# Kernel tuning notes

Measured on AMD Instinct MI355X. Metric: run time of the kernel, lower is better.

## Reference

```python
import jax, jax.numpy as jnp
import numpy as np

NUM_EXPERTS = 8
TOP_K = 2
EMB = 1024
HID = 2048


def setup_inputs() -> dict:
    key = jax.random.key(0)
    k1, k2, k3, k4, k5 = jax.random.split(key, 5)
    x = jax.random.normal(k1, (4, 4096, EMB), dtype=jnp.float32)
    router_w = jax.random.normal(k2, (EMB, NUM_EXPERTS), dtype=jnp.float32) * 0.02
    w_gate = jax.random.normal(k3, (NUM_EXPERTS, EMB, HID), dtype=jnp.float32) * 0.02
    w_up = jax.random.normal(k4, (NUM_EXPERTS, EMB, HID), dtype=jnp.float32) * 0.02
    w_down = jax.random.normal(k5, (NUM_EXPERTS, HID, EMB), dtype=jnp.float32) * 0.02
    return {"x": x, "router_w": router_w, "w_gate": w_gate, "w_up": w_up, "w_down": w_down}


def reference(x, router_w, w_gate, w_up, w_down):
    B, S, D = x.shape
    xf = x.reshape(-1, D)                      # [T, D]
    T = xf.shape[0]
    # Router: top-k over expert logits, softmax over the selected logits,
    # scattered back into a dense [T, E] weight matrix (zeros elsewhere).
    logits = xf @ router_w                     # [T, E]
    top_vals, top_idx = jax.lax.top_k(logits, TOP_K)
    top_probs = jax.nn.softmax(top_vals, axis=-1)
    weights = jnp.zeros((T, NUM_EXPERTS), dtype=xf.dtype)
    weights = weights.at[jnp.arange(T)[:, None], top_idx].set(top_probs)
    # Expert combine: since unselected experts have weight 0, summing the
    # weighted dense expert outputs equals the original masked dispatch/combine.
    out = jnp.zeros_like(xf)
    for e in range(NUM_EXPERTS):
        h = jax.nn.silu(xf @ w_gate[e]) * (xf @ w_up[e])   # SwiGLU [T, H]
        out = out + (h @ w_down[e]) * weights[:, e:e + 1]
    return out.reshape(B, S, D)
```

## Files before the change

### kernel.cpp

```cpp
#include <hip/hip_runtime.h>
#include <hip/hip_fp16.h>


#define T_TOK 16384
#define EMB_D 1024
#define HID_D 2048
#define NEXP  8
#define LIST_CAP (2 * T_TOK + 256)

typedef _Float16 f16x8 __attribute__((ext_vector_type(8)));
typedef _Float16 f16x4 __attribute__((ext_vector_type(4)));
typedef float    f32x4 __attribute__((ext_vector_type(4)));

#define GLD16(gp, lp)                                                          \
  __builtin_amdgcn_global_load_lds(                                            \
      (__attribute__((address_space(1))) void*)(void*)(gp),                    \
      (__attribute__((address_space(3))) void*)(lp), 16, 0, 0)

#define VMW(N)  asm volatile("s_waitcnt vmcnt(" #N ")" ::: "memory")
#define LGKM0() asm volatile("s_waitcnt lgkmcnt(0)" ::: "memory")

__global__ __launch_bounds__(256) void router_kernel(
    const float* __restrict__ x, const float* __restrict__ rw,
    _Float16* __restrict__ xh, int* __restrict__ top_idx,
    float2* __restrict__ top_w) {
  int wave = threadIdx.x >> 6, lane = threadIdx.x & 63;
  int tbase = (blockIdx.x * 4 + wave) * 4;

  float acc[4][NEXP];
#pragma unroll
  for (int tok = 0; tok < 4; tok++)
#pragma unroll
    for (int e = 0; e < NEXP; e++) acc[tok][e] = 0.f;

#pragma unroll
  for (int j = 0; j < 4; j++) {
    int d0 = j * 256 + lane * 4;
    const float* wr = rw + (size_t)d0 * NEXP;
    float wrf[4][NEXP];
#pragma unroll
    for (int k = 0; k < 4; k++) {
      float4 a = *(const float4*)(wr + k * NEXP);
      float4 b = *(const float4*)(wr + k * NEXP + 4);
      wrf[k][0] = a.x; wrf[k][1] = a.y; wrf[k][2] = a.z; wrf[k][3] = a.w;
      wrf[k][4] = b.x; wrf[k][5] = b.y; wrf[k][6] = b.z; wrf[k][7] = b.w;
    }
#pragma unroll
    for (int tok = 0; tok < 4; tok++) {
      int t = tbase + tok;
      float4 xv = *(const float4*)(x + (size_t)t * EMB_D + d0);
      float xs[4] = {xv.x, xv.y, xv.z, xv.w};
#pragma unroll
      for (int k = 0; k < 4; k++)
#pragma unroll
        for (int e = 0; e < NEXP; e++) acc[tok][e] += xs[k] * wrf[k][e];
      f16x4 hx;
      hx[0] = (_Float16)xv.x; hx[1] = (_Float16)xv.y;
      hx[2] = (_Float16)xv.z; hx[3] = (_Float16)xv.w;
      *(f16x4*)(xh + (size_t)t * EMB_D + d0) = hx;
    }
  }

#pragma unroll
  for (int off = 32; off > 0; off >>= 1)
#pragma unroll
    for (int tok = 0; tok < 4; tok++)
#pragma unroll
      for (int e = 0; e < NEXP; e++)
        acc[tok][e] += __shfl_xor(acc[tok][e], off, 64);

  if (lane == 0) {
#pragma unroll
    for (int tok = 0; tok < 4; tok++) {
      int t = tbase + tok;
      int i0 = 0; float v0 = acc[tok][0];
#pragma unroll
      for (int e = 1; e < NEXP; e++)
        if (acc[tok][e] > v0) { v0 = acc[tok][e]; i0 = e; }
      int i1 = (i0 == 0) ? 1 : 0; float v1 = acc[tok][i1];
#pragma unroll
      for (int e = 0; e < NEXP; e++)
        if (e != i0 && acc[tok][e] > v1) { v1 = acc[tok][e]; i1 = e; }
      float p = __expf(v1 - v0);
      float inv = 1.f / (1.f + p);
      top_idx[t] = i0 | (i1 << 16);
      top_w[t] = make_float2(inv, p * inv);
    }
  }
}

__global__ __launch_bounds__(256) void hist_kernel(
    const int* __restrict__ top_idx, int* __restrict__ counts) {
  __shared__ int wcnt[4][NEXP];
  int wave = threadIdx.x >> 6, lane = threadIdx.x & 63;
  int t = blockIdx.x * 256 + threadIdx.x;
  int pk = top_idx[t];
  int e0 = pk & 0xffff, e1 = pk >> 16;
#pragma unroll
  for (int e = 0; e < NEXP; e++) {
    unsigned long long m0 = __ballot(e0 == e);
    unsigned long long m1 = __ballot(e1 == e);
    if (lane == 0) wcnt[wave][e] = __popcll(m0) + __popcll(m1);
  }
  __syncthreads();
  if (threadIdx.x < NEXP) {
    int s = wcnt[0][threadIdx.x] + wcnt[1][threadIdx.x] +
            wcnt[2][threadIdx.x] + wcnt[3][threadIdx.x];
    atomicAdd(&counts[threadIdx.x], s);
  }
}

__global__ void scan_kernel(const int* __restrict__ counts,
                            int* __restrict__ offsets, int* __restrict__ cursor) {
  if (threadIdx.x == 0) {
    int s = 0;
    for (int e = 0; e < NEXP; e++) { offsets[e] = s; s += counts[e]; }
  }
  if (threadIdx.x < NEXP) cursor[threadIdx.x] = 0;
}

__global__ __launch_bounds__(256) void build_kernel(
    const int* __restrict__ top_idx, const float2* __restrict__ top_w,
    const int* __restrict__ offsets, int* cursor,
    int* __restrict__ list_token, float* __restrict__ list_w,
    int2* __restrict__ rows) {
  __shared__ int cnt[NEXP];
  __shared__ int basee[NEXP];
  int t = blockIdx.x * 256 + threadIdx.x;
  if (threadIdx.x < NEXP) cnt[threadIdx.x] = 0;
  __syncthreads();
  int pk = top_idx[t];
  float2 w = top_w[t];
  int e0 = pk & 0xffff, e1 = pk >> 16;
  int loc0 = atomicAdd(&cnt[e0], 1);
  int loc1 = atomicAdd(&cnt[e1], 1);
  __syncthreads();
  if (threadIdx.x < NEXP)
    basee[threadIdx.x] = atomicAdd(&cursor[threadIdx.x], cnt[threadIdx.x]);
  __syncthreads();
  int r0 = offsets[e0] + basee[e0] + loc0;
  list_token[r0] = t; list_w[r0] = w.x;
  int r1 = offsets[e1] + basee[e1] + loc1;
  list_token[r1] = t; list_w[r1] = w.y;
  rows[t] = make_int2(r0, r1);
}

__global__ __launch_bounds__(256) void transpose_cvt(
    const float* __restrict__ src, _Float16* __restrict__ dst, int R, int C) {
  __shared__ float tile[32][33];
  size_t mb = (size_t)blockIdx.z * R * C;
  src += mb; dst += mb;
  int c0 = blockIdx.x * 32, r0 = blockIdx.y * 32;
  int tx = threadIdx.x & 31, ty = threadIdx.x >> 5;
#pragma unroll
  for (int j = 0; j < 4; j++)
    tile[ty + j * 8][tx] = src[(size_t)(r0 + ty + j * 8) * C + c0 + tx];
  __syncthreads();
#pragma unroll
  for (int j = 0; j < 4; j++)
    dst[(size_t)(c0 + ty + j * 8) * R + r0 + tx] = (_Float16)tile[tx][ty + j * 8];
}

__global__ __launch_bounds__(512, 2) void gemm1_kernel(
    const _Float16* __restrict__ xh, const _Float16* __restrict__ wg_t,
    const _Float16* __restrict__ wu_t, const int* __restrict__ counts,
    const int* __restrict__ offsets, const int* __restrict__ list_token,
    _Float16* __restrict__ h) {
  int e = blockIdx.z;
  int Ne = counts[e];
  int m0 = blockIdx.y * 256;
  if (m0 >= Ne) return;
  int n0 = blockIdx.x * 128;
  int base = offsets[e];

  __shared__ _Float16 lds_a[2][256 * 64];
  __shared__ _Float16 lds_bg[2][128 * 64];
  __shared__ _Float16 lds_bu[2][128 * 64];

  int wave = threadIdx.x >> 6, lane = threadIdx.x & 63;
  int lsub = lane >> 3;
  int chunk = (lane & 7) ^ lsub;

  const _Float16* ap[4];
#pragma unroll
  for (int j = 0; j < 4; j++) {
    int lr = j * 64 + wave * 8 + lsub;
    int gidx = base + m0 + lr;
    gidx = min(gidx, 2 * T_TOK - 1);
    int tok = list_token[gidx] & (T_TOK - 1);
    ap[j] = xh + (size_t)tok * EMB_D + chunk * 8;
  }
  const _Float16* bgp[2]; const _Float16* bup[2];
#pragma unroll
  for (int j = 0; j < 2; j++) {
    int nr = n0 + j * 64 + wave * 8 + lsub;
    bgp[j] = wg_t + ((size_t)e * HID_D + nr) * EMB_D + chunk * 8;
    bup[j] = wu_t + ((size_t)e * HID_D + nr) * EMB_D + chunk * 8;
  }

  auto st_a_mh0 = [&](int t, int b) {
    GLD16(ap[0] + t * 64, &lds_a[b][(0 * 64 + wave * 8) * 64]);
    GLD16(ap[2] + t * 64, &lds_a[b][(2 * 64 + wave * 8) * 64]);
  };
  auto st_a_mh1 = [&](int t, int b) {
    GLD16(ap[1] + t * 64, &lds_a[b][(1 * 64 + wave * 8) * 64]);
    GLD16(ap[3] + t * 64, &lds_a[b][(3 * 64 + wave * 8) * 64]);
  };
  auto st_bg = [&](int t, int b) {
    GLD16(bgp[0] + t * 64, &lds_bg[b][(0 * 64 + wave * 8) * 64]);
    GLD16(bgp[1] + t * 64, &lds_bg[b][(1 * 64 + wave * 8) * 64]);
  };
  auto st_bu = [&](int t, int b) {
    GLD16(bup[0] + t * 64, &lds_bu[b][(0 * 64 + wave * 8) * 64]);
    GLD16(bup[1] + t * 64, &lds_bu[b][(1 * 64 + wave * 8) * 64]);
  };

  f32x4 accg[8][2], accu[8][2];
#pragma unroll
  for (int im = 0; im < 8; im++)
#pragma unroll
    for (int in = 0; in < 2; in++) {
      accg[im][in] = (f32x4){0.f, 0.f, 0.f, 0.f};
      accu[im][in] = (f32x4){0.f, 0.f, 0.f, 0.f};
    }

  int wm = (wave >> 2) * 128, wn = (wave & 3) * 32;
  int frow = lane & 15, fquad = lane >> 4;
  int r7 = frow & 7;

  f16x8 af0[4][2], af1[4][2], bgf[2][2], bff[2][2];

#define RD_A(dst, mh, bi)                                                      \
  _Pragma("unroll") for (int im = 0; im < 4; im++)                             \
  _Pragma("unroll") for (int ks = 0; ks < 2; ks++) {                           \
    int rr = wm + (mh) * 64 + im * 16 + frow;                                  \
    int cc = ks * 4 + fquad;                                                   \
    dst[im][ks] = *(const f16x8*)&lds_a[bi][rr * 64 + (((cc) ^ r7) << 3)];     \
  }
#define RD_B(dst, ldsb, bi)                                                    \
  _Pragma("unroll") for (int in = 0; in < 2; in++)                             \
  _Pragma("unroll") for (int ks = 0; ks < 2; ks++) {                           \
    int rr = wn + in * 16 + frow;                                              \
    int cc = ks * 4 + fquad;                                                   \
    dst[in][ks] = *(const f16x8*)&ldsb[bi][rr * 64 + (((cc) ^ r7) << 3)];      \
  }
#define MM16(afr, bfr, acc, mh)                                                \
  __builtin_amdgcn_s_setprio(1);                                               \
  _Pragma("unroll") for (int im = 0; im < 4; im++)                             \
  _Pragma("unroll") for (int in = 0; in < 2; in++)                             \
  _Pragma("unroll") for (int ks = 0; ks < 2; ks++)                             \
    acc[(mh) * 4 + im][in] = __builtin_amdgcn_mfma_f32_16x16x32_f16(           \
        afr[im][ks], bfr[in][ks], acc[(mh) * 4 + im][in], 0, 0, 0);            \
  __builtin_amdgcn_s_setprio(0);

  st_a_mh0(0, 0); st_bg(0, 0); st_bu(0, 0); st_a_mh1(0, 0);
  VMW(0);
  __builtin_amdgcn_s_barrier();

  for (int t = 0; t < 15; ++t) {
    int bi = t & 1;
    RD_A(af0, 0, bi); RD_B(bgf, lds_bg, bi);
    st_a_mh0(t + 1, bi ^ 1);
    __builtin_amdgcn_s_barrier();
    MM16(af0, bgf, accg, 0);
    VMW(4);
    __builtin_amdgcn_s_barrier();
    RD_B(bff, lds_bu, bi);
    st_bg(t + 1, bi ^ 1);
    __builtin_amdgcn_s_barrier();
    MM16(af0, bff, accu, 0);
    VMW(4);
    __builtin_amdgcn_s_barrier();
    RD_A(af1, 1, bi);
    st_bu(t + 1, bi ^ 1);
    __builtin_amdgcn_s_barrier();
    MM16(af1, bgf, accg, 1);
    VMW(4);
    __builtin_amdgcn_s_barrier();
    st_a_mh1(t + 1, bi ^ 1);
    __builtin_amdgcn_s_barrier();
    MM16(af1, bff, accu, 1);
    VMW(4);
    __builtin_amdgcn_s_barrier();
    __builtin_amdgcn_sched_barrier(0);
  }
  {
    const int bi = 1;
    RD_A(af0, 0, bi); RD_B(bgf, lds_bg, bi);
    __builtin_amdgcn_s_barrier();
    MM16(af0, bgf, accg, 0);
    VMW(2);
    __builtin_amdgcn_s_barrier();
    RD_B(bff, lds_bu, bi);
    __builtin_amdgcn_s_barrier();
    MM16(af0, bff, accu, 0);
    VMW(0);
    __builtin_amdgcn_s_barrier();
    RD_A(af1, 1, bi);
    MM16(af1, bgf, accg, 1);
    MM16(af1, bff, accu, 1);
  }
#undef RD_A
#undef RD_B
#undef MM16

#pragma unroll
  for (int im = 0; im < 8; im++)
#pragma unroll
    for (int in = 0; in < 2; in++)
#pragma unroll
      for (int r = 0; r < 4; r++) {
        int lm = m0 + wm + im * 16 + fquad * 4 + r;
        if (lm < Ne) {
          int col = n0 + wn + in * 16 + frow;
          float g = accg[im][in][r], u = accu[im][in][r];
          float hv = (g / (1.f + __expf(-g))) * u;
          h[(size_t)(base + lm) * HID_D + col] = (_Float16)hv;
        }
      }
}

__global__ __launch_bounds__(512) void gemm2_kernel(
    const _Float16* __restrict__ h, const _Float16* __restrict__ wd_t,
    const int* __restrict__ counts, const int* __restrict__ offsets,
    const float* __restrict__ list_w, _Float16* __restrict__ y) {
  int e = blockIdx.z;
  int Ne = counts[e];
  int m0 = blockIdx.y * 256;
  if (m0 >= Ne) return;
  int n0 = blockIdx.x * 256;
  int base = offsets[e];

  __shared__ _Float16 lds_a[2][256 * 64];
  __shared__ _Float16 lds_b[2][256 * 64];

  int wave = threadIdx.x >> 6, lane = threadIdx.x & 63;
  int lsub = lane >> 3;
  int chunk = (lane & 7) ^ lsub;

  const _Float16* ap[4]; const _Float16* bp[4];
#pragma unroll
  for (int j = 0; j < 4; j++) {
    int lr = j * 64 + wave * 8 + lsub;
    ap[j] = h + (size_t)(base + m0 + lr) * HID_D + chunk * 8;
    bp[j] = wd_t + ((size_t)e * EMB_D + n0 + lr) * HID_D + chunk * 8;
  }

  auto stage = [&](int t, int b) {
#pragma unroll
    for (int j = 0; j < 4; j++)
      GLD16(ap[j] + t * 64, &lds_a[b][(j * 64 + wave * 8) * 64]);
#pragma unroll
    for (int j = 0; j < 4; j++)
      GLD16(bp[j] + t * 64, &lds_b[b][(j * 64 + wave * 8) * 64]);
  };

  f32x4 acc[8][4];
#pragma unroll
  for (int im = 0; im < 8; im++)
#pragma unroll
    for (int in = 0; in < 4; in++) acc[im][in] = (f32x4){0.f, 0.f, 0.f, 0.f};

  int wm = (wave >> 2) * 128, wn = (wave & 3) * 64;
  int frow = lane & 15, fquad = lane >> 4;
  int r7 = frow & 7;

  stage(0, 0);
  VMW(0);
  __builtin_amdgcn_s_barrier();

  int cur = 0;
  for (int t = 0; t < 32; ++t) {
    if (t + 1 < 32) stage(t + 1, cur ^ 1);
#pragma unroll
    for (int ks = 0; ks < 2; ++ks) {
      int c = ks * 4 + fquad;
      int sw = ((c ^ r7) << 3);
      f16x8 bf[4], af[8];
#pragma unroll
      for (int in = 0; in < 4; in++)
        bf[in] = *(const f16x8*)&lds_b[cur][(wn + in * 16 + frow) * 64 + sw];
#pragma unroll
      for (int im = 0; im < 8; im++)
        af[im] = *(const f16x8*)&lds_a[cur][(wm + im * 16 + frow) * 64 + sw];
#pragma unroll
      for (int im = 0; im < 8; im++)
#pragma unroll
        for (int in = 0; in < 4; in++)
          acc[im][in] = __builtin_amdgcn_mfma_f32_16x16x32_f16(
              af[im], bf[in], acc[im][in], 0, 0, 0);
    }
    VMW(0);
    LGKM0();
    __builtin_amdgcn_s_barrier();
    cur ^= 1;
  }

#pragma unroll
  for (int im = 0; im < 8; im++)
#pragma unroll
    for (int r = 0; r < 4; r++) {
      int lm = m0 + wm + im * 16 + fquad * 4 + r;
      if (lm < Ne) {
        int gi = base + lm;
        float w = list_w[gi];
#pragma unroll
        for (int in = 0; in < 4; in++) {
          int col = n0 + wn + in * 16 + frow;
          y[(size_t)gi * EMB_D + col] = (_Float16)(acc[im][in][r] * w);
        }
      }
    }
}

__global__ __launch_bounds__(256) void combine_kernel(
    const _Float16* __restrict__ y, const int2* __restrict__ rows,
    float* __restrict__ out) {
  int tid = blockIdx.x * 256 + threadIdx.x;
  int t = tid >> 7;
  int d0 = (tid & 127) * 8;
  int2 r = rows[t];
  f16x8 a = *(const f16x8*)(y + (size_t)r.x * EMB_D + d0);
  f16x8 b = *(const f16x8*)(y + (size_t)r.y * EMB_D + d0);
  float o[8];
#pragma unroll
  for (int j = 0; j < 8; j++) o[j] = (float)a[j] + (float)b[j];
  float* op = out + (size_t)t * EMB_D + d0;
  *(float4*)(op)     = make_float4(o[0], o[1], o[2], o[3]);
  *(float4*)(op + 4) = make_float4(o[4], o[5], o[6], o[7]);
}

extern "C" void kernel_launch(void* const* d_in, const int* in_sizes, int n_in,
                              void* d_out, int out_size, void* d_ws, size_t ws_size,
                              hipStream_t stream) {
  const float* x  = (const float*)d_in[0];
  const float* rw = (const float*)d_in[1];
  const float* wg = (const float*)d_in[2];
  const float* wu = (const float*)d_in[3];
  const float* wd = (const float*)d_in[4];
  float* out = (float*)d_out;

  char* ws = (char*)d_ws;
  size_t off = 0;
  auto alloc = [&](size_t bytes) -> void* {
    void* p = ws + off;
    off += (bytes + 255) & ~(size_t)255;
    return p;
  };
  int*    counts     = (int*)alloc(NEXP * 4);
  int*    cursor     = (int*)alloc(NEXP * 4);
  int*    offsets    = (int*)alloc(NEXP * 4);
  int*    top_idx    = (int*)alloc((size_t)T_TOK * 4);
  float2* top_w      = (float2*)alloc((size_t)T_TOK * 8);
  int*    list_token = (int*)alloc((size_t)LIST_CAP * 4);
  float*  list_w     = (float*)alloc((size_t)LIST_CAP * 4);
  int2*   rows       = (int2*)alloc((size_t)T_TOK * 8);
  _Float16* xh   = (_Float16*)alloc((size_t)T_TOK * EMB_D * 2);
  _Float16* wg_t = (_Float16*)alloc((size_t)NEXP * HID_D * EMB_D * 2);
  _Float16* wu_t = (_Float16*)alloc((size_t)NEXP * HID_D * EMB_D * 2);
  _Float16* wd_t = (_Float16*)alloc((size_t)NEXP * EMB_D * HID_D * 2);
  _Float16* h    = (_Float16*)alloc((size_t)LIST_CAP * HID_D * 2);
  _Float16* y = xh;

  hipMemsetAsync(counts, 0, NEXP * 4, stream);

  router_kernel<<<T_TOK / 16, 256, 0, stream>>>(x, rw, xh, top_idx, top_w);
  hist_kernel<<<T_TOK / 256, 256, 0, stream>>>(top_idx, counts);
  transpose_cvt<<<dim3(HID_D / 32, EMB_D / 32, NEXP), 256, 0, stream>>>(wg, wg_t, EMB_D, HID_D);
  transpose_cvt<<<dim3(HID_D / 32, EMB_D / 32, NEXP), 256, 0, stream>>>(wu, wu_t, EMB_D, HID_D);
  transpose_cvt<<<dim3(EMB_D / 32, HID_D / 32, NEXP), 256, 0, stream>>>(wd, wd_t, HID_D, EMB_D);
  scan_kernel<<<1, 64, 0, stream>>>(counts, offsets, cursor);
  build_kernel<<<T_TOK / 256, 256, 0, stream>>>(top_idx, top_w, offsets, cursor,
                                                list_token, list_w, rows);
  gemm1_kernel<<<dim3(HID_D / 128, T_TOK / 256, NEXP), 512, 0, stream>>>(
      xh, wg_t, wu_t, counts, offsets, list_token, h);
  gemm2_kernel<<<dim3(EMB_D / 256, T_TOK / 256, NEXP), 512, 0, stream>>>(
      h, wd_t, counts, offsets, list_w, y);
  combine_kernel<<<T_TOK * 128 / 256, 256, 0, stream>>>(y, rows, out);
}
```

Measured before the change: 899.3 us.

## Restructure down-projection GEMM into fine-grained interleaved load/MFMA pipeline

The down-projection GEMM's single per-iteration stage-then-compute loop is replaced by four phases, the same scheme the gate/up GEMM already uses. Each phase issues a quarter of the next tile's global-to-LDS loads, then runs one half-M by half-K block of MFMAs at raised priority, separated by barriers and partial vmcnt waits. The aim is to overlap memory traffic with matrix math and shrink the live fragment registers. It also adds a launch-bounds occupancy hint of 2 blocks. That hint caps registers against a 128-float accumulator tile, so spills are a risk, and LDS use may not allow two blocks to co-reside anyway.

New measurement: 856.5 us. 4.8% less time.

```diff
diff --git a/kernel.cpp b/kernel.cpp
--- a/kernel.cpp
+++ b/kernel.cpp
@@ -18,7 +18,7 @@
       (__attribute__((address_space(3))) void*)(lp), 16, 0, 0)
 
 #define VMW(N)  asm volatile("s_waitcnt vmcnt(" #N ")" ::: "memory")
-#define LGKM0() asm volatile("s_waitcnt lgkmcnt(0)" ::: "memory")
+#define BAR()   __builtin_amdgcn_s_barrier()
 
 __global__ __launch_bounds__(256) void router_kernel(
     const float* __restrict__ x, const float* __restrict__ rw,
@@ -255,47 +255,47 @@
 
   st_a_mh0(0, 0); st_bg(0, 0); st_bu(0, 0); st_a_mh1(0, 0);
   VMW(0);
-  __builtin_amdgcn_s_barrier();
+  BAR();
 
   for (int t = 0; t < 15; ++t) {
     int bi = t & 1;
     RD_A(af0, 0, bi); RD_B(bgf, lds_bg, bi);
     st_a_mh0(t + 1, bi ^ 1);
-    __builtin_amdgcn_s_barrier();
+    BAR();
     MM16(af0, bgf, accg, 0);
     VMW(4);
-    __builtin_amdgcn_s_barrier();
+    BAR();
     RD_B(bff, lds_bu, bi);
     st_bg(t + 1, bi ^ 1);
-    __builtin_amdgcn_s_barrier();
+    BAR();
     MM16(af0, bff, accu, 0);
     VMW(4);
-    __builtin_amdgcn_s_barrier();
+    BAR();
     RD_A(af1, 1, bi);
     st_bu(t + 1, bi ^ 1);
-    __builtin_amdgcn_s_barrier();
+    BAR();
     MM16(af1, bgf, accg, 1);
     VMW(4);
-    __builtin_amdgcn_s_barrier();
+    BAR();
     st_a_mh1(t + 1, bi ^ 1);
-    __builtin_amdgcn_s_barrier();
+    BAR();
     MM16(af1, bff, accu, 1);
     VMW(4);
-    __builtin_amdgcn_s_barrier();
+    BAR();
     __builtin_amdgcn_sched_barrier(0);
   }
   {
     const int bi = 1;
     RD_A(af0, 0, bi); RD_B(bgf, lds_bg, bi);
-    __builtin_amdgcn_s_barrier();
+    BAR();
     MM16(af0, bgf, accg, 0);
     VMW(2);
-    __builtin_amdgcn_s_barrier();
+    BAR();
     RD_B(bff, lds_bu, bi);
-    __builtin_amdgcn_s_barrier();
+    BAR();
     MM16(af0, bff, accu, 0);
     VMW(0);
-    __builtin_amdgcn_s_barrier();
+    BAR();
     RD_A(af1, 1, bi);
     MM16(af1, bgf, accg, 1);
     MM16(af1, bff, accu, 1);
@@ -320,7 +320,7 @@
       }
 }
 
-__global__ __launch_bounds__(512) void gemm2_kernel(
+__global__ __launch_bounds__(512, 2) void gemm2_kernel(
     const _Float16* __restrict__ h, const _Float16* __restrict__ wd_t,
     const int* __restrict__ counts, const int* __restrict__ offsets,
     const float* __restrict__ list_w, _Float16* __restrict__ y) {
@@ -346,13 +346,21 @@
     bp[j] = wd_t + ((size_t)e * EMB_D + n0 + lr) * HID_D + chunk * 8;
   }
 
-  auto stage = [&](int t, int b) {
-#pragma unroll
-    for (int j = 0; j < 4; j++)
-      GLD16(ap[j] + t * 64, &lds_a[b][(j * 64 + wave * 8) * 64]);
-#pragma unroll
-    for (int j = 0; j < 4; j++)
-      GLD16(bp[j] + t * 64, &lds_b[b][(j * 64 + wave * 8) * 64]);
+  auto st_a_mh0 = [&](int t, int b) {
+    GLD16(ap[0] + t * 64, &lds_a[b][(0 * 64 + wave * 8) * 64]);
+    GLD16(ap[2] + t * 64, &lds_a[b][(2 * 64 + wave * 8) * 64]);
+  };
+  auto st_a_mh1 = [&](int t, int b) {
+    GLD16(ap[1] + t * 64, &lds_a[b][(1 * 64 + wave * 8) * 64]);
+    GLD16(ap[3] + t * 64, &lds_a[b][(3 * 64 + wave * 8) * 64]);
+  };
+  auto st_b01 = [&](int t, int b) {
+    GLD16(bp[0] + t * 64, &lds_b[b][(0 * 64 + wave * 8) * 64]);
+    GLD16(bp[1] + t * 64, &lds_b[b][(1 * 64 + wave * 8) * 64]);
+  };
+  auto st_b23 = [&](int t, int b) {
+    GLD16(bp[2] + t * 64, &lds_b[b][(2 * 64 + wave * 8) * 64]);
+    GLD16(bp[3] + t * 64, &lds_b[b][(3 * 64 + wave * 8) * 64]);
   };
 
   f32x4 acc[8][4];
@@ -365,36 +373,75 @@
   int frow = lane & 15, fquad = lane >> 4;
   int r7 = frow & 7;
 
-  stage(0, 0);
+  f16x8 af0[4], af1[4], bf[4];
+
+#define RD_A2(dst, mh, ks, bi)                                                 \
+  _Pragma("unroll") for (int im = 0; im < 4; im++) {                           \
+    int rr = wm + (mh) * 64 + im * 16 + frow;                                  \
+    int cc = (ks) * 4 + fquad;                                                 \
+    dst[im] = *(const f16x8*)&lds_a[bi][rr * 64 + (((cc) ^ r7) << 3)];         \
+  }
+#define RD_B2(ks, bi)                                                          \
+  _Pragma("unroll") for (int in = 0; in < 4; in++) {                           \
+    int rr = wn + in * 16 + frow;                                              \
+    int cc = (ks) * 4 + fquad;                                                 \
+    bf[in] = *(const f16x8*)&lds_b[bi][rr * 64 + (((cc) ^ r7) << 3)];          \
+  }
+#define MM16B(afr, mh)                                                         \
+  __builtin_amdgcn_s_setprio(1);                                               \
+  _Pragma("unroll") for (int im = 0; im < 4; im++)                             \
+  _Pragma("unroll") for (int in = 0; in < 4; in++)                             \
+    acc[(mh) * 4 + im][in] = __builtin_amdgcn_mfma_f32_16x16x32_f16(           \
+        afr[im], bf[in], acc[(mh) * 4 + im][in], 0, 0, 0);                     \
+  __builtin_amdgcn_s_setprio(0);
+
+  st_a_mh0(0, 0); st_b01(0, 0); st_b23(0, 0); st_a_mh1(0, 0);
   VMW(0);
-  __builtin_amdgcn_s_barrier();
-
-  int cur = 0;
-  for (int t = 0; t < 32; ++t) {
-    if (t + 1 < 32) stage(t + 1, cur ^ 1);
-#pragma unroll
-    for (int ks = 0; ks < 2; ++ks) {
-      int c = ks * 4 + fquad;
-      int sw = ((c ^ r7) << 3);
-      f16x8 bf[4], af[8];
-#pragma unroll
-      for (int in = 0; in < 4; in++)
-        bf[in] = *(const f16x8*)&lds_b[cur][(wn + in * 16 + frow) * 64 + sw];
-#pragma unroll
-      for (int im = 0; im < 8; im++)
-        af[im] = *(const f16x8*)&lds_a[cur][(wm + im * 16 + frow) * 64 + sw];
-#pragma unroll
-      for (int im = 0; im < 8; im++)
-#pragma unroll
-        for (int in = 0; in < 4; in++)
-          acc[im][in] = __builtin_amdgcn_mfma_f32_16x16x32_f16(
-              af[im], bf[in], acc[im][in], 0, 0, 0);
-    }
+  BAR();
+
+  for (int t = 0; t < 31; ++t) {
+    int bi = t & 1;
+    RD_A2(af0, 0, 0, bi); RD_B2(0, bi);
+    st_a_mh0(t + 1, bi ^ 1);
+    BAR();
+    MM16B(af0, 0);
+    VMW(2);
+    BAR();
+    RD_A2(af1, 1, 0, bi);
+    st_b01(t + 1, bi ^ 1);
+    BAR();
+    MM16B(af1, 1);
+    BAR();
+    RD_A2(af0, 0, 1, bi); RD_B2(1, bi);
+    st_b23(t + 1, bi ^ 1);
+    BAR();
+    MM16B(af0, 0);
+    BAR();
+    RD_A2(af1, 1, 1, bi);
+    st_a_mh1(t + 1, bi ^ 1);
+    BAR();
+    MM16B(af1, 1);
+    VMW(2);
+    BAR();
+    __builtin_amdgcn_sched_barrier(0);
+  }
+  {
+    const int bi = 1;
+    RD_A2(af0, 0, 0, bi); RD_B2(0, bi);
+    BAR();
+    MM16B(af0, 0);
     VMW(0);
-    LGKM0();
-    __builtin_amdgcn_s_barrier();
-    cur ^= 1;
-  }
+    BAR();
+    RD_A2(af1, 1, 0, bi);
+    MM16B(af1, 1);
+    RD_A2(af0, 0, 1, bi); RD_B2(1, bi);
+    MM16B(af0, 0);
+    RD_A2(af1, 1, 1, bi);
+    MM16B(af1, 1);
+  }
+#undef RD_A2
+#undef RD_B2
+#undef MM16B
 
 #pragma unroll
   for (int im = 0; im < 8; im++)
```
